# Kernel tuning notes

Hardware: AMD Instinct MI355X
Metric: run time of the kernel (lower is better)

## Reference

```python
import jax, jax.numpy as jnp
import numpy as np
import itertools

N_SUBSETS = 4
TAU = 0.1


def setup_inputs() -> dict:
    key = jax.random.key(0)
    k1, k2, k3 = jax.random.split(key, 3)
    # scale projections so exp(sim/tau) stays numerically sane (module assumes small/normalized projections)
    projections = jax.random.normal(k1, (8192, 128), dtype=jnp.float32) * 0.05
    xrecon = jax.random.normal(k2, (8192, 784), dtype=jnp.float32)
    recon_label = jax.random.normal(k3, (8192, 784), dtype=jnp.float32)
    return {"projections": projections, "xrecon": xrecon, "recon_label": recon_label}


def _joint_loss(projections, xrecon, recon_label):
    # reconstruction MSE
    recon_loss = jnp.mean(jnp.square(xrecon - recon_label))

    # ---- XNegloss (SimCLR-style with n_subsets positives per group) ----
    N, D = projections.shape
    sim = (projections @ projections.T) / TAU  # [N, N] dot similarity
    gid = jnp.arange(N) // N_SUBSETS
    pos_mask = gid[:, None] == gid[None, :]  # same-group entries are positives
    exp_sim = jnp.exp(sim)
    # original code drops positive entries exactly equal to 1 (positives[positives != 1])
    pos_sum = jnp.sum(jnp.where(pos_mask & (sim != 1.0), exp_sim, 0.0), axis=-1)
    neg_sum = jnp.sum(jnp.where(pos_mask, 0.0, exp_sim), axis=-1)
    closs = jnp.mean(-jnp.log(pos_sum / (pos_sum + neg_sum)))

    # ---- distance loss: MSE over all subset pairs within each group ----
    combi = np.array(list(itertools.combinations(range(N_SUBSETS), 2)))
    left, right = combi[:, 0], combi[:, 1]
    P = projections.reshape(N // N_SUBSETS, N_SUBSETS, D)
    # per-group mean over (pairs, D) then mean over groups == global mean (equal counts)
    dist_loss = jnp.mean(jnp.square(P[:, left] - P[:, right]))

    loss = recon_loss + closs + dist_loss
    return loss, closs, recon_loss, dist_loss


def reference(projections, xrecon, recon_label):
    return _joint_loss(projections, xrecon, recon_label)
```

## Files before the change

kernel.cpp:

```cpp
#include <hip/hip_runtime.h>
#include <hip/hip_bf16.h>
#include <stdint.h>

typedef __bf16 bf16x8 __attribute__((ext_vector_type(8)));
typedef float  f32x4  __attribute__((ext_vector_type(4)));

#define NROWS   8192
#define DIMK    128
#define NGROUPS 2048
#define RECON_N 6422528
#define RECON_N4 (RECON_N / 4)
#define RECON_BLOCKS 1024
#define GROUP_BLOCKS (NGROUPS / 4)

#define WS_SP     0
#define WS_G      (WS_SP + 8 * NROWS)
#define WS_E      (WS_G + NROWS)
#define WS_RPART  (WS_E + NROWS)
#define WS_DPART  (WS_RPART + RECON_BLOCKS)
#define WS_PB     (WS_DPART + GROUP_BLOCKS)

__device__ __forceinline__ void async16(const void* g, void* l) {
    __builtin_amdgcn_global_load_lds(
        (const __attribute__((address_space(1))) void*)g,
        (__attribute__((address_space(3))) void*)l, 16, 0, 0);
}

__device__ __forceinline__ unsigned short f2bf(float f) {
    union { __hip_bfloat16 h; unsigned short u; } v;
    v.h = __float2bfloat16(f);
    return v.u;
}

__global__ __launch_bounds__(256) void convert_kernel(const float4* __restrict__ P,
                                                      uint2* __restrict__ out) {
    int idx = blockIdx.x * 256 + threadIdx.x;
    float4 a = P[idx];
    uint2 r;
    r.x = (uint32_t)f2bf(a.x) | ((uint32_t)f2bf(a.y) << 16);
    r.y = (uint32_t)f2bf(a.z) | ((uint32_t)f2bf(a.w) << 16);
    out[idx] = r;
}

__global__ __launch_bounds__(256) void recon_kernel(const float4* __restrict__ x,
                                                    const float4* __restrict__ y,
                                                    float* __restrict__ rpart) {
    __shared__ float red[4];
    float s = 0.f;
    for (int i = blockIdx.x * 256 + threadIdx.x; i < RECON_N4; i += 256 * RECON_BLOCKS) {
        float4 a = x[i], b = y[i];
        float d0 = a.x - b.x, d1 = a.y - b.y, d2 = a.z - b.z, d3 = a.w - b.w;
        s += d0 * d0 + d1 * d1 + d2 * d2 + d3 * d3;
    }
#pragma unroll
    for (int m = 1; m < 64; m <<= 1) s += __shfl_xor(s, m, 64);
    int wave = threadIdx.x >> 6, lane = threadIdx.x & 63;
    if (lane == 0) red[wave] = s;
    __syncthreads();
    if (threadIdx.x == 0)
        rpart[blockIdx.x] = red[0] + red[1] + red[2] + red[3];
}

__global__ __launch_bounds__(256) void group_kernel(const float* __restrict__ P,
                                                    float* __restrict__ G,
                                                    float* __restrict__ E,
                                                    float* __restrict__ dpart) {
    __shared__ float dred[4];
    int wave = threadIdx.x >> 6, lane = threadIdx.x & 63;
    int g = blockIdx.x * 4 + wave;
    const float* base = P + (size_t)g * 4 * DIMK;
    float v[4][2];
#pragma unroll
    for (int r = 0; r < 4; ++r) {
        v[r][0] = base[r * DIMK + lane];
        v[r][1] = base[r * DIMK + 64 + lane];
    }
    float d[4][4];
#pragma unroll
    for (int r = 0; r < 4; ++r)
#pragma unroll
        for (int s = r; s < 4; ++s) {
            float p = v[r][0] * v[s][0] + v[r][1] * v[s][1];
#pragma unroll
            for (int m = 1; m < 64; m <<= 1) p += __shfl_xor(p, m, 64);
            d[r][s] = p; d[s][r] = p;
        }
    if (lane == 0) {
        float distp = 0.f;
#pragma unroll
        for (int r = 0; r < 4; ++r)
#pragma unroll
            for (int s = r + 1; s < 4; ++s)
                distp += d[r][r] + d[s][s] - 2.f * d[r][s];
        dred[wave] = distp;
#pragma unroll
        for (int r = 0; r < 4; ++r) {
            float Gs = 0.f, Es = 0.f;
#pragma unroll
            for (int s = 0; s < 4; ++s) {
                float sim = d[r][s] * 10.0f;
                float e = __expf(sim);
                Gs += e;
                if (sim == 1.0f) Es += e;
            }
            G[g * 4 + r] = Gs;
            E[g * 4 + r] = Es;
        }
    }
    __syncthreads();
    if (threadIdx.x == 0)
        dpart[blockIdx.x] = dred[0] + dred[1] + dred[2] + dred[3];
}

__global__ __launch_bounds__(256, 2) void sim_kernel(const unsigned short* __restrict__ P,
                                                     float* __restrict__ Sp) {
    __shared__ unsigned short tile[128 * 128];
    __shared__ float sred[2][2][64];
    const int wave = threadIdx.x >> 6, lane = threadIdx.x & 63;
    const int wr = wave >> 1, wc = wave & 1;
    const int rowBase = blockIdx.x * 128;
    const int colBase = blockIdx.y * 1024;

    {
        const char* g = (const char*)(P + (size_t)rowBase * DIMK);
#pragma unroll
        for (int i = 0; i < 8; ++i) {
            int seg = i * 4 + wave;
            async16(g + seg * 1024 + lane * 16, (char*)tile + seg * 1024);
        }
    }
    __syncthreads();

    bf16x8 Af[4][4];
    {
        int m = lane & 15, kq = lane >> 4;
#pragma unroll
        for (int i = 0; i < 4; ++i) {
            const unsigned short* rowp = tile + (wr * 64 + i * 16 + m) * 128 + kq * 8;
#pragma unroll
            for (int kk = 0; kk < 4; ++kk)
                Af[i][kk] = *(const bf16x8*)(rowp + kk * 32);
        }
    }
    __syncthreads();

    float rowAcc[4][4];
#pragma unroll
    for (int i = 0; i < 4; ++i)
#pragma unroll
        for (int r = 0; r < 4; ++r) rowAcc[i][r] = 0.f;

    for (int t = 0; t < 8; ++t) {
        {
            const char* g = (const char*)(P + (size_t)(colBase + t * 128) * DIMK);
#pragma unroll
            for (int i = 0; i < 8; ++i) {
                int seg = i * 4 + wave;
                async16(g + seg * 1024 + lane * 16, (char*)tile + seg * 1024);
            }
        }
        __syncthreads();

        f32x4 acc[4][4];
#pragma unroll
        for (int i = 0; i < 4; ++i)
#pragma unroll
            for (int j = 0; j < 4; ++j) acc[i][j] = (f32x4){0.f, 0.f, 0.f, 0.f};

        int n = lane & 15, kq = lane >> 4;
#pragma unroll
        for (int kk = 0; kk < 4; ++kk) {
            bf16x8 Bf[4];
#pragma unroll
            for (int j = 0; j < 4; ++j)
                Bf[j] = *(const bf16x8*)(tile + (wc * 64 + j * 16 + n) * 128 + kq * 8 + kk * 32);
#pragma unroll
            for (int i = 0; i < 4; ++i)
#pragma unroll
                for (int j = 0; j < 4; ++j)
                    acc[i][j] = __builtin_amdgcn_mfma_f32_16x16x32_bf16(Af[i][kk], Bf[j], acc[i][j], 0, 0, 0);
        }
#pragma unroll
        for (int i = 0; i < 4; ++i)
#pragma unroll
            for (int j = 0; j < 4; ++j)
#pragma unroll
                for (int r = 0; r < 4; ++r)
                    rowAcc[i][r] += __expf(acc[i][j][r] * 10.0f);
        __syncthreads();
    }

#pragma unroll
    for (int i = 0; i < 4; ++i)
#pragma unroll
        for (int r = 0; r < 4; ++r) {
            float sv = rowAcc[i][r];
            sv += __shfl_xor(sv, 1, 64);
            sv += __shfl_xor(sv, 2, 64);
            sv += __shfl_xor(sv, 4, 64);
            sv += __shfl_xor(sv, 8, 64);
            rowAcc[i][r] = sv;
        }
    if ((lane & 15) == 0) {
        int c = lane >> 4;
#pragma unroll
        for (int i = 0; i < 4; ++i)
#pragma unroll
            for (int r = 0; r < 4; ++r)
                sred[wc][wr][i * 16 + c * 4 + r] = rowAcc[i][r];
    }
    __syncthreads();
    if (wc == 0) {
        float v = sred[0][wr][lane] + sred[1][wr][lane];
        Sp[(size_t)blockIdx.y * NROWS + rowBase + wr * 64 + lane] = v;
    }
}

__global__ __launch_bounds__(256) void finalize_kernel(const float* __restrict__ ws,
                                                       float* __restrict__ out) {
    const float* Sp    = ws + WS_SP;
    const float* G     = ws + WS_G;
    const float* E     = ws + WS_E;
    const float* rpart = ws + WS_RPART;
    const float* dpart = ws + WS_DPART;
    __shared__ float redc[4], redr[4], redd[4];

    float c = 0.f;
    for (int r = threadIdx.x; r < NROWS; r += 256) {
        float Sv = 0.f;
#pragma unroll
        for (int q = 0; q < 8; ++q) Sv += Sp[q * NROWS + r];
        c += __logf(Sv - E[r]) - __logf(G[r] - E[r]);
    }
    float rs = 0.f;
    for (int i = threadIdx.x; i < RECON_BLOCKS; i += 256) rs += rpart[i];
    float ds = 0.f;
    for (int i = threadIdx.x; i < GROUP_BLOCKS; i += 256) ds += dpart[i];

#pragma unroll
    for (int m = 1; m < 64; m <<= 1) {
        c  += __shfl_xor(c,  m, 64);
        rs += __shfl_xor(rs, m, 64);
        ds += __shfl_xor(ds, m, 64);
    }
    int wave = threadIdx.x >> 6, lane = threadIdx.x & 63;
    if (lane == 0) { redc[wave] = c; redr[wave] = rs; redd[wave] = ds; }
    __syncthreads();
    if (threadIdx.x == 0) {
        float closs = (redc[0] + redc[1] + redc[2] + redc[3]) / (float)NROWS;
        float recon = (redr[0] + redr[1] + redr[2] + redr[3]) / (float)RECON_N;
        float dist  = (redd[0] + redd[1] + redd[2] + redd[3]) / (float)(NGROUPS * 6 * DIMK);
        float loss  = recon + closs + dist;
        out[0] = loss;
        out[1] = closs;
        out[2] = recon;
        out[3] = dist;
    }
}

extern "C" void kernel_launch(void* const* d_in, const int* in_sizes, int n_in,
                              void* d_out, int out_size, void* d_ws, size_t ws_size,
                              hipStream_t stream) {
    const float* P  = (const float*)d_in[0];
    const float4* X = (const float4*)d_in[1];
    const float4* Y = (const float4*)d_in[2];
    float* out = (float*)d_out;
    float* w = (float*)d_ws;
    unsigned short* Pb = (unsigned short*)(w + WS_PB);

    convert_kernel<<<NROWS * DIMK / 4 / 256, 256, 0, stream>>>((const float4*)P, (uint2*)Pb);
    recon_kernel<<<RECON_BLOCKS, 256, 0, stream>>>(X, Y, w + WS_RPART);
    group_kernel<<<GROUP_BLOCKS, 256, 0, stream>>>(P, w + WS_G, w + WS_E, w + WS_DPART);
    sim_kernel<<<dim3(64, 8), 256, 0, stream>>>(Pb, w + WS_SP);
    finalize_kernel<<<1, 256, 0, stream>>>(w, out);
}
```

Measured before the change: 135.0 us.

## Fuse sim, recon and group kernels into one heterogeneous launch

Merges the similarity GEMM, reconstruction MSE and group-loss kernels into one grid whose blocks branch by index, so the memory-bound recon work can overlap the MFMA-bound sim work. The sim path drops LDS tiling and reads B fragments straight from global memory through cache, and uses exp2f with a folded constant. Recon blocks now each handle a fixed chunk without a loop. The single-block finalize is split into a 32-block closs reduction plus a tiny combine kernel. This risks more global load traffic in the GEMM and adds one extra launch.

```diff
diff --git a/kernel.cpp b/kernel.cpp
--- a/kernel.cpp
+++ b/kernel.cpp
@@ -10,21 +10,21 @@
 #define NGROUPS 2048
 #define RECON_N 6422528
 #define RECON_N4 (RECON_N / 4)
-#define RECON_BLOCKS 1024
+#define SIM_BLOCKS   512
+#define RECON_BLOCKS 1568
 #define GROUP_BLOCKS (NGROUPS / 4)
+#define FUSED_BLOCKS (SIM_BLOCKS + RECON_BLOCKS + GROUP_BLOCKS)
+#define CLOSS_BLOCKS 32
+
+#define LOG2E10 14.4269504088896341f
 
 #define WS_SP     0
-#define WS_G      (WS_SP + 8 * NROWS)
-#define WS_E      (WS_G + NROWS)
-#define WS_RPART  (WS_E + NROWS)
-#define WS_DPART  (WS_RPART + RECON_BLOCKS)
-#define WS_PB     (WS_DPART + GROUP_BLOCKS)
-
-__device__ __forceinline__ void async16(const void* g, void* l) {
-    __builtin_amdgcn_global_load_lds(
-        (const __attribute__((address_space(1))) void*)g,
-        (__attribute__((address_space(3))) void*)l, 16, 0, 0);
-}
+#define WS_G      65536
+#define WS_E      73728
+#define WS_RPART  81920
+#define WS_DPART  83488
+#define WS_CPART  84000
+#define WS_PB     84032
 
 __device__ __forceinline__ unsigned short f2bf(float f) {
     union { __hip_bfloat16 h; unsigned short u; } v;
@@ -42,216 +42,206 @@
     out[idx] = r;
 }
 
-__global__ __launch_bounds__(256) void recon_kernel(const float4* __restrict__ x,
-                                                    const float4* __restrict__ y,
-                                                    float* __restrict__ rpart) {
+__global__ __launch_bounds__(256, 2) void fused_kernel(
+        const unsigned short* __restrict__ Pb,
+        const float* __restrict__ Pf,
+        const float4* __restrict__ X,
+        const float4* __restrict__ Y,
+        float* __restrict__ ws) {
+    const int bx = blockIdx.x;
+    const int wave = threadIdx.x >> 6, lane = threadIdx.x & 63;
+
+    if (bx < SIM_BLOCKS) {
+        float* Sp = ws + WS_SP;
+        __shared__ float sred[2][2][64];
+        const int wr = wave >> 1, wc = wave & 1;
+        const int rowBase = (bx >> 3) * 128;
+        const int colBase = (bx & 7) * 1024;
+        const int m = lane & 15, kq = lane >> 4;
+
+        bf16x8 Af[4][4];
+#pragma unroll
+        for (int i = 0; i < 4; ++i) {
+            const unsigned short* rowp =
+                Pb + (size_t)(rowBase + wr * 64 + i * 16 + m) * DIMK + kq * 8;
+#pragma unroll
+            for (int kk = 0; kk < 4; ++kk)
+                Af[i][kk] = *(const bf16x8*)(rowp + kk * 32);
+        }
+
+        float rowAcc[4][4];
+#pragma unroll
+        for (int i = 0; i < 4; ++i)
+#pragma unroll
+            for (int r = 0; r < 4; ++r) rowAcc[i][r] = 0.f;
+
+        for (int t = 0; t < 8; ++t) {
+            const unsigned short* bbase =
+                Pb + (size_t)(colBase + t * 128 + wc * 64) * DIMK;
+#pragma unroll
+            for (int j = 0; j < 4; ++j) {
+                const unsigned short* bp = bbase + (j * 16 + m) * DIMK + kq * 8;
+                bf16x8 Bf[4];
+#pragma unroll
+                for (int kk = 0; kk < 4; ++kk)
+                    Bf[kk] = *(const bf16x8*)(bp + kk * 32);
+                f32x4 acc[4];
+#pragma unroll
+                for (int i = 0; i < 4; ++i) acc[i] = (f32x4){0.f, 0.f, 0.f, 0.f};
+#pragma unroll
+                for (int kk = 0; kk < 4; ++kk)
+#pragma unroll
+                    for (int i = 0; i < 4; ++i)
+                        acc[i] = __builtin_amdgcn_mfma_f32_16x16x32_bf16(
+                            Af[i][kk], Bf[kk], acc[i], 0, 0, 0);
+#pragma unroll
+                for (int i = 0; i < 4; ++i)
+#pragma unroll
+                    for (int r = 0; r < 4; ++r)
+                        rowAcc[i][r] += exp2f(acc[i][r] * LOG2E10);
+            }
+        }
+
+#pragma unroll
+        for (int i = 0; i < 4; ++i)
+#pragma unroll
+            for (int r = 0; r < 4; ++r) {
+                float sv = rowAcc[i][r];
+                sv += __shfl_xor(sv, 1, 64);
+                sv += __shfl_xor(sv, 2, 64);
+                sv += __shfl_xor(sv, 4, 64);
+                sv += __shfl_xor(sv, 8, 64);
+                rowAcc[i][r] = sv;
+            }
+        if ((lane & 15) == 0) {
+            int c = lane >> 4;
+#pragma unroll
+            for (int i = 0; i < 4; ++i)
+#pragma unroll
+                for (int r = 0; r < 4; ++r)
+                    sred[wc][wr][i * 16 + c * 4 + r] = rowAcc[i][r];
+        }
+        __syncthreads();
+        if (wc == 0) {
+            float v = sred[0][wr][lane] + sred[1][wr][lane];
+            Sp[(size_t)(bx & 7) * NROWS + rowBase + wr * 64 + lane] = v;
+        }
+    } else if (bx < SIM_BLOCKS + RECON_BLOCKS) {
+        __shared__ float red[4];
+        int rb = bx - SIM_BLOCKS;
+        int base = rb * 1024 + threadIdx.x;
+        float4 a0 = X[base], b0 = Y[base];
+        float4 a1 = X[base + 256], b1 = Y[base + 256];
+        float4 a2 = X[base + 512], b2 = Y[base + 512];
+        float4 a3 = X[base + 768], b3 = Y[base + 768];
+        float s = 0.f;
+        float d;
+        d = a0.x - b0.x; s += d * d;  d = a0.y - b0.y; s += d * d;
+        d = a0.z - b0.z; s += d * d;  d = a0.w - b0.w; s += d * d;
+        d = a1.x - b1.x; s += d * d;  d = a1.y - b1.y; s += d * d;
+        d = a1.z - b1.z; s += d * d;  d = a1.w - b1.w; s += d * d;
+        d = a2.x - b2.x; s += d * d;  d = a2.y - b2.y; s += d * d;
+        d = a2.z - b2.z; s += d * d;  d = a2.w - b2.w; s += d * d;
+        d = a3.x - b3.x; s += d * d;  d = a3.y - b3.y; s += d * d;
+        d = a3.z - b3.z; s += d * d;  d = a3.w - b3.w; s += d * d;
+#pragma unroll
+        for (int mm = 1; mm < 64; mm <<= 1) s += __shfl_xor(s, mm, 64);
+        if (lane == 0) red[wave] = s;
+        __syncthreads();
+        if (threadIdx.x == 0)
+            ws[WS_RPART + rb] = red[0] + red[1] + red[2] + red[3];
+    } else {
+        __shared__ float dred[4];
+        float* G = ws + WS_G;
+        float* E = ws + WS_E;
+        int gb = bx - (SIM_BLOCKS + RECON_BLOCKS);
+        int g = gb * 4 + wave;
+        const float* base = Pf + (size_t)g * 4 * DIMK;
+        float v[4][2];
+#pragma unroll
+        for (int r = 0; r < 4; ++r) {
+            v[r][0] = base[r * DIMK + lane];
+            v[r][1] = base[r * DIMK + 64 + lane];
+        }
+        float dmat[4][4];
+#pragma unroll
+        for (int r = 0; r < 4; ++r)
+#pragma unroll
+            for (int s2 = r; s2 < 4; ++s2) {
+                float p = v[r][0] * v[s2][0] + v[r][1] * v[s2][1];
+#pragma unroll
+                for (int mm = 1; mm < 64; mm <<= 1) p += __shfl_xor(p, mm, 64);
+                dmat[r][s2] = p; dmat[s2][r] = p;
+            }
+        if (lane == 0) {
+            float distp = 0.f;
+#pragma unroll
+            for (int r = 0; r < 4; ++r)
+#pragma unroll
+                for (int s2 = r + 1; s2 < 4; ++s2)
+                    distp += dmat[r][r] + dmat[s2][s2] - 2.f * dmat[r][s2];
+            dred[wave] = distp;
+#pragma unroll
+            for (int r = 0; r < 4; ++r) {
+                float Gs = 0.f, Es = 0.f;
+#pragma unroll
+                for (int s2 = 0; s2 < 4; ++s2) {
+                    float sim = dmat[r][s2] * 10.0f;
+                    float e = __expf(sim);
+                    Gs += e;
+                    if (sim == 1.0f) Es += e;
+                }
+                G[g * 4 + r] = Gs;
+                E[g * 4 + r] = Es;
+            }
+        }
+        __syncthreads();
+        if (threadIdx.x == 0)
+            ws[WS_DPART + gb] = dred[0] + dred[1] + dred[2] + dred[3];
+    }
+}
+
+__global__ __launch_bounds__(256) void closs_kernel(const float* __restrict__ ws,
+                                                    float* __restrict__ cpart) {
     __shared__ float red[4];
-    float s = 0.f;
-    for (int i = blockIdx.x * 256 + threadIdx.x; i < RECON_N4; i += 256 * RECON_BLOCKS) {
-        float4 a = x[i], b = y[i];
-        float d0 = a.x - b.x, d1 = a.y - b.y, d2 = a.z - b.z, d3 = a.w - b.w;
-        s += d0 * d0 + d1 * d1 + d2 * d2 + d3 * d3;
-    }
-#pragma unroll
-    for (int m = 1; m < 64; m <<= 1) s += __shfl_xor(s, m, 64);
+    const float* Sp = ws + WS_SP;
+    const float* G  = ws + WS_G;
+    const float* E  = ws + WS_E;
+    int r = blockIdx.x * 256 + threadIdx.x;
+    float Sv = 0.f;
+#pragma unroll
+    for (int q = 0; q < 8; ++q) Sv += Sp[q * NROWS + r];
+    float c = __logf(Sv - E[r]) - __logf(G[r] - E[r]);
+#pragma unroll
+    for (int m = 1; m < 64; m <<= 1) c += __shfl_xor(c, m, 64);
     int wave = threadIdx.x >> 6, lane = threadIdx.x & 63;
-    if (lane == 0) red[wave] = s;
+    if (lane == 0) red[wave] = c;
     __syncthreads();
     if (threadIdx.x == 0)
-        rpart[blockIdx.x] = red[0] + red[1] + red[2] + red[3];
-}
-
-__global__ __launch_bounds__(256) void group_kernel(const float* __restrict__ P,
-                                                    float* __restrict__ G,
-                                                    float* __restrict__ E,
-                                                    float* __restrict__ dpart) {
-    __shared__ float dred[4];
-    int wave = threadIdx.x >> 6, lane = threadIdx.x & 63;
-    int g = blockIdx.x * 4 + wave;
-    const float* base = P + (size_t)g * 4 * DIMK;
-    float v[4][2];
-#pragma unroll
-    for (int r = 0; r < 4; ++r) {
-        v[r][0] = base[r * DIMK + lane];
-        v[r][1] = base[r * DIMK + 64 + lane];
-    }
-    float d[4][4];
-#pragma unroll
-    for (int r = 0; r < 4; ++r)
-#pragma unroll
-        for (int s = r; s < 4; ++s) {
-            float p = v[r][0] * v[s][0] + v[r][1] * v[s][1];
-#pragma unroll
-            for (int m = 1; m < 64; m <<= 1) p += __shfl_xor(p, m, 64);
-            d[r][s] = p; d[s][r] = p;
-        }
-    if (lane == 0) {
-        float distp = 0.f;
-#pragma unroll
-        for (int r = 0; r < 4; ++r)
-#pragma unroll
-            for (int s = r + 1; s < 4; ++s)
-                distp += d[r][r] + d[s][s] - 2.f * d[r][s];
-        dred[wave] = distp;
-#pragma unroll
-        for (int r = 0; r < 4; ++r) {
-            float Gs = 0.f, Es = 0.f;
-#pragma unroll
-            for (int s = 0; s < 4; ++s) {
-                float sim = d[r][s] * 10.0f;
-                float e = __expf(sim);
-                Gs += e;
-                if (sim == 1.0f) Es += e;
-            }
-            G[g * 4 + r] = Gs;
-            E[g * 4 + r] = Es;
-        }
-    }
-    __syncthreads();
-    if (threadIdx.x == 0)
-        dpart[blockIdx.x] = dred[0] + dred[1] + dred[2] + dred[3];
-}
-
-__global__ __launch_bounds__(256, 2) void sim_kernel(const unsigned short* __restrict__ P,
-                                                     float* __restrict__ Sp) {
-    __shared__ unsigned short tile[128 * 128];
-    __shared__ float sred[2][2][64];
-    const int wave = threadIdx.x >> 6, lane = threadIdx.x & 63;
-    const int wr = wave >> 1, wc = wave & 1;
-    const int rowBase = blockIdx.x * 128;
-    const int colBase = blockIdx.y * 1024;
-
-    {
-        const char* g = (const char*)(P + (size_t)rowBase * DIMK);
-#pragma unroll
-        for (int i = 0; i < 8; ++i) {
-            int seg = i * 4 + wave;
-            async16(g + seg * 1024 + lane * 16, (char*)tile + seg * 1024);
-        }
-    }
-    __syncthreads();
-
-    bf16x8 Af[4][4];
-    {
-        int m = lane & 15, kq = lane >> 4;
-#pragma unroll
-        for (int i = 0; i < 4; ++i) {
-            const unsigned short* rowp = tile + (wr * 64 + i * 16 + m) * 128 + kq * 8;
-#pragma unroll
-            for (int kk = 0; kk < 4; ++kk)
-                Af[i][kk] = *(const bf16x8*)(rowp + kk * 32);
-        }
-    }
-    __syncthreads();
-
-    float rowAcc[4][4];
-#pragma unroll
-    for (int i = 0; i < 4; ++i)
-#pragma unroll
-        for (int r = 0; r < 4; ++r) rowAcc[i][r] = 0.f;
-
-    for (int t = 0; t < 8; ++t) {
-        {
-            const char* g = (const char*)(P + (size_t)(colBase + t * 128) * DIMK);
-#pragma unroll
-            for (int i = 0; i < 8; ++i) {
-                int seg = i * 4 + wave;
-                async16(g + seg * 1024 + lane * 16, (char*)tile + seg * 1024);
-            }
-        }
-        __syncthreads();
-
-        f32x4 acc[4][4];
-#pragma unroll
-        for (int i = 0; i < 4; ++i)
-#pragma unroll
-            for (int j = 0; j < 4; ++j) acc[i][j] = (f32x4){0.f, 0.f, 0.f, 0.f};
-
-        int n = lane & 15, kq = lane >> 4;
-#pragma unroll
-        for (int kk = 0; kk < 4; ++kk) {
-            bf16x8 Bf[4];
-#pragma unroll
-            for (int j = 0; j < 4; ++j)
-                Bf[j] = *(const bf16x8*)(tile + (wc * 64 + j * 16 + n) * 128 + kq * 8 + kk * 32);
-#pragma unroll
-            for (int i = 0; i < 4; ++i)
-#pragma unroll
-                for (int j = 0; j < 4; ++j)
-                    acc[i][j] = __builtin_amdgcn_mfma_f32_16x16x32_bf16(Af[i][kk], Bf[j], acc[i][j], 0, 0, 0);
-        }
-#pragma unroll
-        for (int i = 0; i < 4; ++i)
-#pragma unroll
-            for (int j = 0; j < 4; ++j)
-#pragma unroll
-                for (int r = 0; r < 4; ++r)
-                    rowAcc[i][r] += __expf(acc[i][j][r] * 10.0f);
-        __syncthreads();
-    }
-
-#pragma unroll
-    for (int i = 0; i < 4; ++i)
-#pragma unroll
-        for (int r = 0; r < 4; ++r) {
-            float sv = rowAcc[i][r];
-            sv += __shfl_xor(sv, 1, 64);
-            sv += __shfl_xor(sv, 2, 64);
-            sv += __shfl_xor(sv, 4, 64);
-            sv += __shfl_xor(sv, 8, 64);
-            rowAcc[i][r] = sv;
-        }
-    if ((lane & 15) == 0) {
-        int c = lane >> 4;
-#pragma unroll
-        for (int i = 0; i < 4; ++i)
-#pragma unroll
-            for (int r = 0; r < 4; ++r)
-                sred[wc][wr][i * 16 + c * 4 + r] = rowAcc[i][r];
-    }
-    __syncthreads();
-    if (wc == 0) {
-        float v = sred[0][wr][lane] + sred[1][wr][lane];
-        Sp[(size_t)blockIdx.y * NROWS + rowBase + wr * 64 + lane] = v;
-    }
-}
-
-__global__ __launch_bounds__(256) void finalize_kernel(const float* __restrict__ ws,
-                                                       float* __restrict__ out) {
-    const float* Sp    = ws + WS_SP;
-    const float* G     = ws + WS_G;
-    const float* E     = ws + WS_E;
-    const float* rpart = ws + WS_RPART;
-    const float* dpart = ws + WS_DPART;
+        cpart[blockIdx.x] = red[0] + red[1] + red[2] + red[3];
+}
+
+__global__ __launch_bounds__(256) void combine_kernel(const float* __restrict__ ws,
+                                                      float* __restrict__ out) {
     __shared__ float redc[4], redr[4], redd[4];
-
-    float c = 0.f;
-    for (int r = threadIdx.x; r < NROWS; r += 256) {
-        float Sv = 0.f;
-#pragma unroll
-        for (int q = 0; q < 8; ++q) Sv += Sp[q * NROWS + r];
-        c += __logf(Sv - E[r]) - __logf(G[r] - E[r]);
-    }
-    float rs = 0.f;
-    for (int i = threadIdx.x; i < RECON_BLOCKS; i += 256) rs += rpart[i];
-    float ds = 0.f;
-    for (int i = threadIdx.x; i < GROUP_BLOCKS; i += 256) ds += dpart[i];
-
+    float cs = 0.f, rs = 0.f, ds = 0.f;
+    for (int i = threadIdx.x; i < CLOSS_BLOCKS; i += 256) cs += ws[WS_CPART + i];
+    for (int i = threadIdx.x; i < RECON_BLOCKS; i += 256) rs += ws[WS_RPART + i];
+    for (int i = threadIdx.x; i < GROUP_BLOCKS; i += 256) ds += ws[WS_DPART + i];
 #pragma unroll
     for (int m = 1; m < 64; m <<= 1) {
-        c  += __shfl_xor(c,  m, 64);
+        cs += __shfl_xor(cs, m, 64);
         rs += __shfl_xor(rs, m, 64);
         ds += __shfl_xor(ds, m, 64);
     }
     int wave = threadIdx.x >> 6, lane = threadIdx.x & 63;
-    if (lane == 0) { redc[wave] = c; redr[wave] = rs; redd[wave] = ds; }
+    if (lane == 0) { redc[wave] = cs; redr[wave] = rs; redd[wave] = ds; }
     __syncthreads();
     if (threadIdx.x == 0) {
         float closs = (redc[0] + redc[1] + redc[2] + redc[3]) / (float)NROWS;
         float recon = (redr[0] + redr[1] + redr[2] + redr[3]) / (float)RECON_N;
         float dist  = (redd[0] + redd[1] + redd[2] + redd[3]) / (float)(NGROUPS * 6 * DIMK);
-        float loss  = recon + closs + dist;
-        out[0] = loss;
+        out[0] = recon + closs + dist;
         out[1] = closs;
         out[2] = recon;
         out[3] = dist;
@@ -269,8 +259,7 @@
     unsigned short* Pb = (unsigned short*)(w + WS_PB);
 
     convert_kernel<<<NROWS * DIMK / 4 / 256, 256, 0, stream>>>((const float4*)P, (uint2*)Pb);
-    recon_kernel<<<RECON_BLOCKS, 256, 0, stream>>>(X, Y, w + WS_RPART);
-    group_kernel<<<GROUP_BLOCKS, 256, 0, stream>>>(P, w + WS_G, w + WS_E, w + WS_DPART);
-    sim_kernel<<<dim3(64, 8), 256, 0, stream>>>(Pb, w + WS_SP);
-    finalize_kernel<<<1, 256, 0, stream>>>(w, out);
-}
+    fused_kernel<<<FUSED_BLOCKS, 256, 0, stream>>>(Pb, P, X, Y, w);
+    closs_kernel<<<CLOSS_BLOCKS, 256, 0, stream>>>(w, w + WS_CPART);
+    combine_kernel<<<1, 256, 0, stream>>>(w, out);
+}
```

Result: faster. 126.2 us (-6.5%).
